# Kernel tuning notes

Measured on AMD Instinct MI355X. Metric: run time of the kernel, lower is better.

The kernel has to match this reference:

```python
import jax, jax.numpy as jnp
import numpy as np

N = 10000
E = 160000
IN_CH, HID, OUT = 14, 128, 4
HEADS = 8
NEG_SLOPE = 0.2


def setup_inputs() -> dict:
    key = jax.random.key(0)
    ks = jax.random.split(key, 16)
    glorot = lambda k, shape: jax.random.normal(k, shape, jnp.float32) * np.sqrt(2.0 / (shape[0] + shape[-1]))
    inp = {
        'x': jax.random.normal(ks[0], (N, IN_CH), jnp.float32),
        'edge_index': jax.random.randint(ks[1], (2, E), 0, N, jnp.int64),
        # layer 1: 14 -> 8 heads x 128, concat
        'W1': glorot(ks[2], (IN_CH, HEADS * HID)),
        'a_src1': glorot(ks[3], (HEADS, HID)),
        'a_dst1': glorot(ks[4], (HEADS, HID)),
        'b1': jnp.zeros((HEADS * HID,), jnp.float32),
        # layer 2: 1024 -> 8 heads x 128, concat
        'W2': glorot(ks[5], (HEADS * HID, HEADS * HID)),
        'a_src2': glorot(ks[6], (HEADS, HID)),
        'a_dst2': glorot(ks[7], (HEADS, HID)),
        'b2': jnp.zeros((HEADS * HID,), jnp.float32),
        # layer 3: 1024 -> 1 head x 4, mean (concat=False)
        'W3': glorot(ks[8], (HEADS * HID, OUT)),
        'a_src3': glorot(ks[9], (1, OUT)),
        'a_dst3': glorot(ks[10], (1, OUT)),
        'b3': jnp.zeros((OUT,), jnp.float32),
    }
    return inp


def gat_conv(x, src, dst, W, a_src, a_dst, b, heads, out_ch, concat):
    n = x.shape[0]
    h = (x @ W).reshape(n, heads, out_ch)                      # [N,H,C]
    al_s = jnp.sum(h * a_src, axis=-1)                         # [N,H]
    al_d = jnp.sum(h * a_dst, axis=-1)                         # [N,H]
    e = al_s[src] + al_d[dst]                                  # [E,H]
    e = jnp.where(e > 0, e, NEG_SLOPE * e)                     # LeakyReLU(0.2)
    # segment softmax over incoming edges of each dst node
    m = jax.ops.segment_max(e, dst, num_segments=n)
    ex = jnp.exp(e - m[dst])
    z = jax.ops.segment_sum(ex, dst, num_segments=n)
    alpha = ex / (z[dst] + 1e-16)                              # [E,H]
    out = jax.ops.segment_sum(h[src] * alpha[:, :, None], dst, num_segments=n)  # [N,H,C]
    out = out.reshape(n, heads * out_ch) if concat else out.mean(axis=1)
    return out + b


def reference(x, edge_index, W1, a_src1, a_dst1, b1, W2, a_src2, a_dst2, b2, W3, a_src3, a_dst3, b3):
    n = x.shape[0]
    # add self-loops (PyG GATConv default)
    loop = jnp.arange(n, dtype=edge_index.dtype)
    src = jnp.concatenate([edge_index[0], loop])
    dst = jnp.concatenate([edge_index[1], loop])
    # dropout layers are identity in eval mode
    h = gat_conv(x, src, dst, W1, a_src1, a_dst1, b1, HEADS, HID, True)
    h = jax.nn.relu(h)
    h = gat_conv(h, src, dst, W2, a_src2, a_dst2, b2, HEADS, HID, True)
    h = jax.nn.relu(h)
    h = gat_conv(h, src, dst, W3, a_src3, a_dst3, b3, 1, OUT, False)
    h = jax.nn.relu(h)
    return h
```

## Files before the change

### kernel.cpp

```cpp
#include <hip/hip_runtime.h>

typedef unsigned short ushort_t;
typedef unsigned int uint32;

#define N_NODES 10000
#define N_EDGES 160000
#define ET (N_NODES + N_EDGES)
#define HT 1024
#define HEADS 8
#define NEG 0.2f

#define O_FLAG     0
#define O_BND      64
#define O_COUNTS   256
#define O_OFFS     (O_COUNTS + 40192)
#define O_SSORT    (O_OFFS + 40192)
#define O_ALS1     (O_SSORT + 680192)
#define O_ALD1     (O_ALS1 + 320000)
#define O_ALS2     (O_ALD1 + 320000)
#define O_ALD2     (O_ALS2 + 320000)
#define O_AL3S     O_ALS2
#define O_AL3D     (O_ALS2 + 40192)
#define O_H3       (O_ALS2 + 80384)
#define O_WVEC     (O_ALD2 + 320000)
#define O_W3F      (O_WVEC + 24576)
#define O_S3F      (O_W3F + 16384)
#define O_W2T      (O_S3F + 768)
#define O_BUFA     (O_W2T + 2097152)
#define O_BUFB     (O_BUFA + 20480000)

__device__ __forceinline__ float bf2f(ushort_t u){ return __uint_as_float(((uint32)u) << 16); }
__device__ __forceinline__ ushort_t f2bf(float f){
    uint32 x = __float_as_uint(f);
    return (ushort_t)((x + 0x7fffu + ((x >> 16) & 1u)) >> 16);
}
__device__ __forceinline__ void unpack2(uint32 u, float& lo, float& hi){
    lo = __uint_as_float(u << 16);
    hi = __uint_as_float(u & 0xffff0000u);
}

typedef __bf16 bf16x8 __attribute__((ext_vector_type(8)));
typedef float  f32x4  __attribute__((ext_vector_type(4)));

typedef const __attribute__((address_space(1))) uint32* gas1_u32;
typedef       __attribute__((address_space(3))) uint32* las3_u32;

__device__ __forceinline__ void gload_lds16(const void* g, void* l){
    __builtin_amdgcn_global_load_lds((gas1_u32)g, (las3_u32)l, 16, 0, 0);
}

__device__ __forceinline__ int probe_f32(const uint32* __restrict__ w){
    int cnt = 0;
    for (int i = 0; i < 256; i++){
        uint32 e = (w[i] >> 7) & 0xffu;
        cnt += (e >= 64u && e <= 160u) ? 1 : 0;
    }
    return (cnt > 200) ? 0 : 1;
}
__global__ void k_probe(const int* __restrict__ ei, const uint32* __restrict__ w1raw,
                        int* __restrict__ flags){
    if (threadIdx.x == 0){
        int nz = 0;
        for (int i = 0; i < 128; i++) nz |= ei[2*i + 1];
        flags[0] = (nz == 0) ? 1 : 0;
    }
    if (threadIdx.x == 1) flags[1] = probe_f32(w1raw);
}

__device__ __forceinline__ float cvt1(const void* p, int i, int f32){
    return f32 ? ((const float*)p)[i] : bf2f(((const ushort_t*)p)[i]);
}

struct CvtArgs {
    const void* vsrc[6];
    const void* w3src;
    const void* s3src[3];
};

__global__ __launch_bounds__(256) void k_setup(CvtArgs a, const void* __restrict__ W2,
                                               const int* __restrict__ flags,
                                               float* __restrict__ wvecF, float* __restrict__ W3F,
                                               float* __restrict__ s3F,
                                               int* __restrict__ counts,
                                               float* __restrict__ alS2, float* __restrict__ alD2,
                                               uint32* __restrict__ bnd,
                                               ushort_t* __restrict__ W2T){
    __shared__ ushort_t tile[32][33];
    int b = blockIdx.x, tid = threadIdx.x;
    int f32 = flags[1];
    if (b < 11){
        if (b == 0 && tid < 32) bnd[tid] = 0;
        int g = b * 1024 + tid * 4;
        #pragma unroll
        for (int j = 0; j < 4; j++){
            int i = g + j;
            if (i < 6144) wvecF[i] = cvt1(a.vsrc[i >> 10], i & 1023, f32);
            else if (i < 10240) W3F[i - 6144] = cvt1(a.w3src, i - 6144, f32);
            else if (i < 10252){
                int off = i - 10240;
                s3F[(off >> 2) * 16 + (off & 3)] = cvt1(a.s3src[off >> 2], off & 3, f32);
            }
        }
    } else if (b < 21){
        int g = (b - 11) * 1024 + tid * 4;
        #pragma unroll
        for (int j = 0; j < 4; j++) if (g + j < N_NODES) counts[g + j] = 0;
    } else if (b < 178){
        int g = (b - 21) * 1024 + tid * 4;
        if (g < 80000){ *(float4*)(alS2 + g) = make_float4(0,0,0,0); }
        else if (g < 160000){ *(float4*)(alD2 + g - 80000) = make_float4(0,0,0,0); }
    } else {
        int t = b - 178;
        int bx = t & 31, by = t >> 5;
        int cx = tid & 31, ry = (tid >> 5) * 4;
        #pragma unroll
        for (int r = 0; r < 4; r++){
            size_t idx = (size_t)(by*32 + ry + r)*1024 + bx*32 + cx;
            tile[ry + r][cx] = f32 ? f2bf(((const float*)W2)[idx]) : ((const ushort_t*)W2)[idx];
        }
        __syncthreads();
        #pragma unroll
        for (int r = 0; r < 4; r++)
            W2T[(size_t)(bx*32 + ry + r)*1024 + by*32 + cx] = tile[cx][ry + r];
    }
}

__global__ __launch_bounds__(256) void k_extract_hist(const void* __restrict__ ei, const int* __restrict__ flags,
                                                      int* __restrict__ counts){
    int i = blockIdx.x * 256 + threadIdx.x;
    int is64 = flags[0];
    int d = -1;
    if (i < N_EDGES){
        d = is64 ? (int)((const long long*)ei)[N_EDGES + i] : ((const int*)ei)[N_EDGES + i];
    } else if (i < ET){
        d = i - N_EDGES;
    }
    if (d >= 0) atomicAdd(&counts[d], 1);
}

__global__ __launch_bounds__(1024) void k_scan(int* __restrict__ counts, int* __restrict__ offs, int n){
    __shared__ int wsum[16];
    __shared__ int running_s;
    int tid = threadIdx.x;
    int lane = tid & 63, wid = tid >> 6;
    if (tid == 0) running_s = 0;
    __syncthreads();
    for (int base = 0; base < n; base += 1024){
        int i = base + tid;
        int v = (i < n) ? counts[i] : 0;
        int x = v;
        #pragma unroll
        for (int d = 1; d < 64; d <<= 1){
            int t = __shfl_up(x, d, 64);
            if (lane >= d) x += t;
        }
        if (lane == 63) wsum[wid] = x;
        __syncthreads();
        if (wid == 0 && lane < 16){
            int w = wsum[lane];
            #pragma unroll
            for (int d = 1; d < 16; d <<= 1){
                int t = __shfl_up(w, d, 64);
                if (lane >= d) w += t;
            }
            wsum[lane] = w;
        }
        __syncthreads();
        int wprefix = (wid == 0) ? 0 : wsum[wid - 1];
        int run = running_s;
        int excl = run + wprefix + (x - v);
        if (i < n){ offs[i] = excl; counts[i] = excl; }
        __syncthreads();
        if (tid == 0) running_s = run + wsum[15];
        __syncthreads();
    }
    if (tid == 0) offs[n] = running_s;
}

__global__ __launch_bounds__(256) void k_scatter(const void* __restrict__ ei, const int* __restrict__ flags,
                                                 int* __restrict__ cursors, int* __restrict__ ssort){
    int i = blockIdx.x * 256 + threadIdx.x;
    if (i >= ET) return;
    int is64 = flags[0];
    int s, d;
    if (i < N_EDGES){
        if (is64){
            s = (int)((const long long*)ei)[i];
            d = (int)((const long long*)ei)[N_EDGES + i];
        } else {
            s = ((const int*)ei)[i];
            d = ((const int*)ei)[N_EDGES + i];
        }
    } else { s = i - N_EDGES; d = s; }
    int pos = atomicAdd(&cursors[d], 1);
    ssort[pos] = s;
}

__global__ __launch_bounds__(256) void k_gemm1f(const void* __restrict__ x, const void* __restrict__ W1,
                                                const int* __restrict__ flags,
                                                const float* __restrict__ wvecF,
                                                ushort_t* __restrict__ h1,
                                                float* __restrict__ alS, float* __restrict__ alD,
                                                uint32* __restrict__ bnd){
    __shared__ float w1s[14 * HT];
    __shared__ uint32 smax[16];
    int tid = threadIdx.x;
    int f32 = flags[1];
    if (tid < 16) smax[tid] = 0;
    if (f32){
        for (int i = tid * 4; i < 14 * HT; i += 1024)
            *(float4*)(w1s + i) = *(const float4*)((const float*)W1 + i);
    } else {
        for (int i = tid * 4; i < 14 * HT; i += 1024){
            uint2 u = *(const uint2*)((const ushort_t*)W1 + i);
            unpack2(u.x, w1s[i], w1s[i+1]);
            unpack2(u.y, w1s[i+2], w1s[i+3]);
        }
    }
    __syncthreads();
    int c0 = tid * 4;
    float4 sv = *(const float4*)(wvecF + c0);
    float4 dv = *(const float4*)(wvecF + 1024 + c0);
    int head = tid >> 5, l32 = tid & 31;
    #pragma unroll 1
    for (int n = blockIdx.x; n < N_NODES; n += 512){
        float a0=0.f, a1=0.f, a2=0.f, a3=0.f;
        #pragma unroll
        for (int k = 0; k < 14; k++){
            float xv = f32 ? ((const float*)x)[n*14 + k] : bf2f(((const ushort_t*)x)[n*14 + k]);
            float4 w = *(const float4*)(w1s + k*HT + c0);
            a0 += xv*w.x; a1 += xv*w.y; a2 += xv*w.z; a3 += xv*w.w;
        }
        uint2 o;
        o.x = (uint32)f2bf(a0) | ((uint32)f2bf(a1) << 16);
        o.y = (uint32)f2bf(a2) | ((uint32)f2bf(a3) << 16);
        *(uint2*)(h1 + (size_t)n*HT + c0) = o;
        float h0,h1v,h2,h3v;
        unpack2(o.x, h0, h1v); unpack2(o.y, h2, h3v);
        float s = h0*sv.x + h1v*sv.y + h2*sv.z + h3v*sv.w;
        float d = h0*dv.x + h1v*dv.y + h2*dv.z + h3v*dv.w;
        #pragma unroll
        for (int of = 16; of; of >>= 1){ s += __shfl_xor(s, of, 32); d += __shfl_xor(d, of, 32); }
        if (l32 == 0){
            alS[n*HEADS + head] = s; alD[n*HEADS + head] = d;
            atomicMax(&smax[head],     __float_as_uint(fmaxf(s, 0.f)));
            atomicMax(&smax[8 + head], __float_as_uint(fmaxf(d, 0.f)));
        }
    }
    __syncthreads();
    if (tid < 16) atomicMax(&bnd[tid], smax[tid]);
}

__global__ __launch_bounds__(256) void k_bound(const float* __restrict__ alS2, const float* __restrict__ alD2,
                                               uint32* __restrict__ bnd){
    int g = blockIdx.x * 256 + threadIdx.x;
    int lane = threadIdx.x & 63;
    float ms = 0.f, md = 0.f;
    for (int i = g; i < 80000; i += 10240){ ms = fmaxf(ms, alS2[i]); md = fmaxf(md, alD2[i]); }
    #pragma unroll
    for (int o = 8; o < 64; o <<= 1){
        ms = fmaxf(ms, __shfl_xor(ms, o, 64));
        md = fmaxf(md, __shfl_xor(md, o, 64));
    }
    if (lane < 8){
        atomicMax(&bnd[16 + lane], __float_as_uint(ms));
        atomicMax(&bnd[24 + lane], __float_as_uint(md));
    }
}

__global__ __launch_bounds__(256) void k_gat_agg(const ushort_t* __restrict__ H, const float* __restrict__ alS,
                                                 const float* __restrict__ alD, const uint32* __restrict__ bnd,
                                                 int bo, const int* __restrict__ offs,
                                                 const int* __restrict__ srcs, const float* __restrict__ bias,
                                                 ushort_t* __restrict__ out){
    int tid = threadIdx.x;
    int wv = tid >> 6, lane = tid & 63;
    int n = blockIdx.x * 2 + (wv >> 1);
    int half = wv & 1;
    int beg = offs[n], end = offs[n+1];
    int head = half*4 + (lane >> 4);
    float ad = alD[n*HEADS + head];
    float B = __uint_as_float(bnd[bo + head]) + __uint_as_float(bnd[bo + 8 + head]);

    int ch0 = half*512 + lane*8;
    const ushort_t* Hc = H + ch0;
    float z = 0.f;
    float c0=0.f,c1=0.f,c2=0.f,c3=0.f,c4=0.f,c5=0.f,c6=0.f,c7=0.f;
    for (int c = beg; c < end; c += 64){
        int cn = min(64, end - c);
        int sreg = (lane < cn) ? srcs[c + lane] : 0;
        int j = 0;
        for (; j + 8 <= cn; j += 8){
            int s[8]; uint4 u[8]; float e[8];
            #pragma unroll
            for (int q = 0; q < 8; q++) s[q] = __shfl(sreg, j + q, 64);
            #pragma unroll
            for (int q = 0; q < 8; q++) u[q] = *(const uint4*)(Hc + (size_t)s[q]*HT);
            #pragma unroll
            for (int q = 0; q < 8; q++) e[q] = alS[s[q]*HEADS + head];
            #pragma unroll
            for (int q = 0; q < 8; q++){
                float v = e[q] + ad;
                v = v > 0.f ? v : NEG*v;
                float w = __expf(v - B);
                z += w;
                float f0,f1,f2,f3,f4,f5,f6,f7;
                unpack2(u[q].x,f0,f1); unpack2(u[q].y,f2,f3);
                unpack2(u[q].z,f4,f5); unpack2(u[q].w,f6,f7);
                c0+=w*f0; c1+=w*f1; c2+=w*f2; c3+=w*f3;
                c4+=w*f4; c5+=w*f5; c6+=w*f6; c7+=w*f7;
            }
        }
        for (; j < cn; j++){
            int s0 = __shfl(sreg, j, 64);
            uint4 u0 = *(const uint4*)(Hc + (size_t)s0*HT);
            float v = alS[s0*HEADS + head] + ad;
            v = v > 0.f ? v : NEG*v;
            float w = __expf(v - B);
            z += w;
            float f0,f1,f2,f3,f4,f5,f6,f7;
            unpack2(u0.x,f0,f1); unpack2(u0.y,f2,f3); unpack2(u0.z,f4,f5); unpack2(u0.w,f6,f7);
            c0+=w*f0; c1+=w*f1; c2+=w*f2; c3+=w*f3;
            c4+=w*f4; c5+=w*f5; c6+=w*f6; c7+=w*f7;
        }
    }
    float inv = 1.f / z;
    float4 b0 = *(const float4*)(bias + ch0);
    float4 b1 = *(const float4*)(bias + ch0 + 4);
    c0 = fmaxf(c0*inv + b0.x, 0.f); c1 = fmaxf(c1*inv + b0.y, 0.f);
    c2 = fmaxf(c2*inv + b0.z, 0.f); c3 = fmaxf(c3*inv + b0.w, 0.f);
    c4 = fmaxf(c4*inv + b1.x, 0.f); c5 = fmaxf(c5*inv + b1.y, 0.f);
    c6 = fmaxf(c6*inv + b1.z, 0.f); c7 = fmaxf(c7*inv + b1.w, 0.f);
    uint4 o;
    o.x = (uint32)f2bf(c0) | ((uint32)f2bf(c1) << 16);
    o.y = (uint32)f2bf(c2) | ((uint32)f2bf(c3) << 16);
    o.z = (uint32)f2bf(c4) | ((uint32)f2bf(c5) << 16);
    o.w = (uint32)f2bf(c6) | ((uint32)f2bf(c7) << 16);
    *(uint4*)(out + (size_t)n*HT + ch0) = o;
}

__global__ __launch_bounds__(256) void k_gemm2(const ushort_t* __restrict__ A, const ushort_t* __restrict__ BT,
                                               ushort_t* __restrict__ C,
                                               const float* __restrict__ aS, const float* __restrict__ aD,
                                               float* __restrict__ alS2, float* __restrict__ alD2){
    __shared__ ushort_t lA[128*64];
    __shared__ ushort_t lB[64*64];
    int bn = blockIdx.x, bm = blockIdx.y;
    int tid = threadIdx.x;
    int lane = tid & 63;
    int wave = tid >> 6;
    int wm = wave * 32;
    int lm = lane & 15, kg = lane >> 4;
    int swz = lm & 7;
    f32x4 acc[2][4];
    #pragma unroll
    for (int i = 0; i < 2; i++)
        #pragma unroll
        for (int j = 0; j < 4; j++) acc[i][j] = (f32x4)0.0f;

    int rowA0 = bm * 128, rowB0 = bn * 64;
    for (int k0 = 0; k0 < 1024; k0 += 64){
        #pragma unroll
        for (int it = 0; it < 4; ++it){
            int s = tid + it*256;
            int r = s >> 3, q = s & 7;
            int ra = rowA0 + r; if (ra > N_NODES-1) ra = N_NODES-1;
            gload_lds16(A + (size_t)ra*1024 + k0 + (q ^ (r & 7))*8, lA + s*8);
        }
        #pragma unroll
        for (int it = 0; it < 2; ++it){
            int s = tid + it*256;
            int r = s >> 3, q = s & 7;
            gload_lds16(BT + (size_t)(rowB0 + r)*1024 + k0 + (q ^ (r & 7))*8, lB + s*8);
        }
        __syncthreads();
        #pragma unroll
        for (int kh = 0; kh < 2; kh++){
            bf16x8 af[2], bfr[4];
            int qb = kh*4 + kg;
            int qp = (qb ^ swz) * 8;
            #pragma unroll
            for (int mt = 0; mt < 2; mt++) af[mt]  = *(const bf16x8*)(lA + (wm + mt*16 + lm)*64 + qp);
            #pragma unroll
            for (int nt = 0; nt < 4; nt++) bfr[nt] = *(const bf16x8*)(lB + (nt*16 + lm)*64 + qp);
            #pragma unroll
            for (int mt = 0; mt < 2; mt++)
                #pragma unroll
                for (int nt = 0; nt < 4; nt++)
                    acc[mt][nt] = __builtin_amdgcn_mfma_f32_16x16x32_bf16(af[mt], bfr[nt], acc[mt][nt], 0, 0, 0);
        }
        __syncthreads();
    }
    #pragma unroll
    for (int mt = 0; mt < 2; mt++){
        int row_base = bm*128 + wm + mt*16 + kg*4;
        #pragma unroll
        for (int nt = 0; nt < 4; nt++){
            int col = bn*64 + nt*16 + lm;
            #pragma unroll
            for (int r = 0; r < 4; r++){
                int row = row_base + r;
                if (row < N_NODES) C[(size_t)row*HT + col] = f2bf(acc[mt][nt][r]);
            }
        }
    }
    int head = bn >> 1;
    float as_l[4], ad_l[4];
    #pragma unroll
    for (int nt = 0; nt < 4; nt++){
        as_l[nt] = aS[bn*64 + nt*16 + lm];
        ad_l[nt] = aD[bn*64 + nt*16 + lm];
    }
    #pragma unroll
    for (int mt = 0; mt < 2; mt++){
        #pragma unroll
        for (int r = 0; r < 4; r++){
            float ps = acc[mt][0][r]*as_l[0] + acc[mt][1][r]*as_l[1]
                     + acc[mt][2][r]*as_l[2] + acc[mt][3][r]*as_l[3];
            float pd = acc[mt][0][r]*ad_l[0] + acc[mt][1][r]*ad_l[1]
                     + acc[mt][2][r]*ad_l[2] + acc[mt][3][r]*ad_l[3];
            #pragma unroll
            for (int o = 1; o < 16; o <<= 1){ ps += __shfl_xor(ps, o, 64); pd += __shfl_xor(pd, o, 64); }
            if (lm == 0){
                int row = bm*128 + wm + mt*16 + kg*4 + r;
                if (row < N_NODES){
                    atomicAdd(&alS2[row*HEADS + head], ps);
                    atomicAdd(&alD2[row*HEADS + head], pd);
                }
            }
        }
    }
}

__global__ __launch_bounds__(256) void k_gemm3(const ushort_t* __restrict__ A, const float* __restrict__ W3,
                                               const float* __restrict__ s3,
                                               float* __restrict__ h3, float* __restrict__ al3s, float* __restrict__ al3d){
    int tid = threadIdx.x;
    int lane = tid & 63, wave = tid >> 6;
    int n = blockIdx.x * 4 + wave;
    if (n >= N_NODES) return;
    float4 w3r[16];
    #pragma unroll
    for (int j = 0; j < 16; j++) w3r[j] = ((const float4*)W3)[lane*16 + j];
    const uint4* ap = (const uint4*)(A + (size_t)n*HT + lane*16);
    uint4 u0 = ap[0], u1 = ap[1];
    uint32 uu[8] = {u0.x,u0.y,u0.z,u0.w,u1.x,u1.y,u1.z,u1.w};
    float acc0=0.f, acc1=0.f, acc2=0.f, acc3=0.f;
    #pragma unroll
    for (int p = 0; p < 8; p++){
        float lo, hi;
        unpack2(uu[p], lo, hi);
        float4 wl = w3r[p*2], wh = w3r[p*2+1];
        acc0 += lo*wl.x + hi*wh.x;
        acc1 += lo*wl.y + hi*wh.y;
        acc2 += lo*wl.z + hi*wh.z;
        acc3 += lo*wl.w + hi*wh.w;
    }
    #pragma unroll
    for (int o = 32; o; o >>= 1){
        acc0 += __shfl_xor(acc0, o, 64); acc1 += __shfl_xor(acc1, o, 64);
        acc2 += __shfl_xor(acc2, o, 64); acc3 += __shfl_xor(acc3, o, 64);
    }
    if (lane == 0){
        *(float4*)(h3 + n*4) = make_float4(acc0, acc1, acc2, acc3);
        al3s[n] = acc0*s3[0] + acc1*s3[1] + acc2*s3[2] + acc3*s3[3];
        al3d[n] = acc0*s3[16] + acc1*s3[17] + acc2*s3[18] + acc3*s3[19];
    }
}

__global__ __launch_bounds__(256) void k_gat_agg3(const float* __restrict__ h3, const float* __restrict__ al3s,
                                                  const float* __restrict__ al3d, const int* __restrict__ offs,
                                                  const int* __restrict__ srcs, const float* __restrict__ b3,
                                                  const int* __restrict__ flags, void* __restrict__ out){
    int tid = threadIdx.x;
    int l = tid & 63, wave = tid >> 6;
    int n = blockIdx.x * 4 + wave;
    if (n >= N_NODES) return;
    int beg = offs[n], end = offs[n+1];
    float ad = al3d[n];
    float m = -1e30f;
    for (int e = beg + l; e < end; e += 64){
        float v = al3s[srcs[e]] + ad; v = v > 0.f ? v : NEG*v;
        m = fmaxf(m, v);
    }
    #pragma unroll
    for (int o = 32; o; o >>= 1) m = fmaxf(m, __shfl_xor(m, o, 64));
    float z = 0.f;
    for (int e = beg + l; e < end; e += 64){
        float v = al3s[srcs[e]] + ad; v = v > 0.f ? v : NEG*v;
        z += __expf(v - m);
    }
    #pragma unroll
    for (int o = 32; o; o >>= 1) z += __shfl_xor(z, o, 64);
    float inv = 1.f / (z + 1e-16f);
    float a0=0.f, a1=0.f, a2=0.f, a3=0.f;
    for (int e = beg + l; e < end; e += 64){
        int s = srcs[e];
        float v = al3s[s] + ad; v = v > 0.f ? v : NEG*v;
        float w = __expf(v - m) * inv;
        float4 hv = *(const float4*)(h3 + s*4);
        a0 += w*hv.x; a1 += w*hv.y; a2 += w*hv.z; a3 += w*hv.w;
    }
    #pragma unroll
    for (int o = 32; o; o >>= 1){
        a0 += __shfl_xor(a0, o, 64); a1 += __shfl_xor(a1, o, 64);
        a2 += __shfl_xor(a2, o, 64); a3 += __shfl_xor(a3, o, 64);
    }
    if (l == 0){
        float r0 = fmaxf(a0 + b3[0], 0.f);
        float r1 = fmaxf(a1 + b3[1], 0.f);
        float r2 = fmaxf(a2 + b3[2], 0.f);
        float r3 = fmaxf(a3 + b3[3], 0.f);
        if (flags[1]){
            float* o4 = (float*)out;
            o4[n*4+0]=r0; o4[n*4+1]=r1; o4[n*4+2]=r2; o4[n*4+3]=r3;
        } else {
            ushort_t* o2 = (ushort_t*)out;
            o2[n*4+0]=f2bf(r0); o2[n*4+1]=f2bf(r1); o2[n*4+2]=f2bf(r2); o2[n*4+3]=f2bf(r3);
        }
    }
}

extern "C" void kernel_launch(void* const* d_in, const int* in_sizes, int n_in,
                              void* d_out, int out_size, void* d_ws, size_t ws_size,
                              hipStream_t stream){
    const void* x   = d_in[0];
    const void* ei  = d_in[1];
    const void* W1  = d_in[2];
    const void* W2  = d_in[6];
    const void* W3  = d_in[10];

    char* ws = (char*)d_ws;
    int* flags     = (int*)(ws + O_FLAG);
    uint32* bnd    = (uint32*)(ws + O_BND);
    int* counts    = (int*)(ws + O_COUNTS);
    int* offs      = (int*)(ws + O_OFFS);
    int* ssort     = (int*)(ws + O_SSORT);
    float* alS1    = (float*)(ws + O_ALS1);
    float* alD1    = (float*)(ws + O_ALD1);
    float* alS2    = (float*)(ws + O_ALS2);
    float* alD2    = (float*)(ws + O_ALD2);
    float* al3s    = (float*)(ws + O_AL3S);
    float* al3d    = (float*)(ws + O_AL3D);
    float* h3      = (float*)(ws + O_H3);
    float* wvecF   = (float*)(ws + O_WVEC);
    float* W3F     = (float*)(ws + O_W3F);
    float* s3F     = (float*)(ws + O_S3F);
    ushort_t* W2T  = (ushort_t*)(ws + O_W2T);
    ushort_t* bufA = (ushort_t*)(ws + O_BUFA);
    ushort_t* bufB = (ushort_t*)(ws + O_BUFB);

    const int EB = (ET + 255) / 256;

    CvtArgs ca;
    ca.vsrc[0]=d_in[3];  ca.vsrc[1]=d_in[4];  ca.vsrc[2]=d_in[5];
    ca.vsrc[3]=d_in[7];  ca.vsrc[4]=d_in[8];  ca.vsrc[5]=d_in[9];
    ca.w3src = W3;
    ca.s3src[0]=d_in[11]; ca.s3src[1]=d_in[12]; ca.s3src[2]=d_in[13];

    k_probe<<<1, 64, 0, stream>>>((const int*)ei, (const uint32*)W1, flags);
    k_setup<<<1202, 256, 0, stream>>>(ca, W2, flags, wvecF, W3F, s3F, counts, alS2, alD2, bnd, W2T);
    k_extract_hist<<<EB, 256, 0, stream>>>(ei, flags, counts);
    k_scan<<<1, 1024, 0, stream>>>(counts, offs, N_NODES);
    k_scatter<<<EB, 256, 0, stream>>>(ei, flags, counts, ssort);

    k_gemm1f<<<512, 256, 0, stream>>>(x, W1, flags, wvecF, bufA, alS1, alD1, bnd);
    k_gat_agg<<<5000, 256, 0, stream>>>(bufA, alS1, alD1, bnd, 0, offs, ssort, wvecF + 2*1024, bufB);

    k_gemm2<<<dim3(16, 79), 256, 0, stream>>>(bufB, W2T, bufA, wvecF + 3*1024, wvecF + 4*1024, alS2, alD2);
    k_bound<<<40, 256, 0, stream>>>(alS2, alD2, bnd);
    k_gat_agg<<<5000, 256, 0, stream>>>(bufA, alS2, alD2, bnd, 16, offs, ssort, wvecF + 5*1024, bufB);

    k_gemm3<<<2500, 256, 0, stream>>>(bufB, W3F, s3F, h3, al3s, al3d);
    k_gat_agg3<<<2500, 256, 0, stream>>>(h3, al3s, al3d, offs, ssort, s3F + 32, flags, d_out);
}
```

Baseline: 342.4 us.

## Fold probe into setup, fuse histogram with gemm1, parallelize scan

Removes the separate probe kernel by computing the dtype and edge-width probes inside k_setup. Merges the degree histogram with the layer-1 projection into one launch using block-index partitioning. Replaces the single-block serial scan with a two-kernel multi-block scan, where each block sums the preceding block totals itself. This cuts launch count and serialization on the CSR build path. The cost is that every setup block re-runs the f32 probe, and the gemm1 blocks now reserve large LDS even when they run alongside the lightweight histogram blocks.

```diff
diff --git a/kernel.cpp b/kernel.cpp
--- a/kernel.cpp
+++ b/kernel.cpp
@@ -12,7 +12,8 @@
 
 #define O_FLAG     0
 #define O_BND      64
-#define O_COUNTS   256
+#define O_BSUM     192
+#define O_COUNTS   512
 #define O_OFFS     (O_COUNTS + 40192)
 #define O_SSORT    (O_OFFS + 40192)
 #define O_ALS1     (O_SSORT + 680192)
@@ -57,14 +58,10 @@
     }
     return (cnt > 200) ? 0 : 1;
 }
-__global__ void k_probe(const int* __restrict__ ei, const uint32* __restrict__ w1raw,
-                        int* __restrict__ flags){
-    if (threadIdx.x == 0){
-        int nz = 0;
-        for (int i = 0; i < 128; i++) nz |= ei[2*i + 1];
-        flags[0] = (nz == 0) ? 1 : 0;
-    }
-    if (threadIdx.x == 1) flags[1] = probe_f32(w1raw);
+__device__ __forceinline__ int probe_edge64(const int* __restrict__ ei){
+    int nz = 0;
+    for (int i = 0; i < 128; i++) nz |= ei[2*i + 1];
+    return (nz == 0) ? 1 : 0;
 }
 
 __device__ __forceinline__ float cvt1(const void* p, int i, int f32){
@@ -78,7 +75,9 @@
 };
 
 __global__ __launch_bounds__(256) void k_setup(CvtArgs a, const void* __restrict__ W2,
-                                               const int* __restrict__ flags,
+                                               const uint32* __restrict__ w1raw,
+                                               const int* __restrict__ eiraw,
+                                               int* __restrict__ flags,
                                                float* __restrict__ wvecF, float* __restrict__ W3F,
                                                float* __restrict__ s3F,
                                                int* __restrict__ counts,
@@ -87,9 +86,13 @@
                                                ushort_t* __restrict__ W2T){
     __shared__ ushort_t tile[32][33];
     int b = blockIdx.x, tid = threadIdx.x;
-    int f32 = flags[1];
+    int f32 = probe_f32(w1raw);
     if (b < 11){
-        if (b == 0 && tid < 32) bnd[tid] = 0;
+        if (b == 0){
+            if (tid < 32) bnd[tid] = 0;
+            if (tid == 32) flags[0] = probe_edge64(eiraw);
+            if (tid == 33) flags[1] = f32;
+        }
         int g = b * 1024 + tid * 4;
         #pragma unroll
         for (int j = 0; j < 4; j++){
@@ -125,56 +128,112 @@
     }
 }
 
-__global__ __launch_bounds__(256) void k_extract_hist(const void* __restrict__ ei, const int* __restrict__ flags,
-                                                      int* __restrict__ counts){
-    int i = blockIdx.x * 256 + threadIdx.x;
-    int is64 = flags[0];
-    int d = -1;
-    if (i < N_EDGES){
-        d = is64 ? (int)((const long long*)ei)[N_EDGES + i] : ((const int*)ei)[N_EDGES + i];
-    } else if (i < ET){
-        d = i - N_EDGES;
-    }
-    if (d >= 0) atomicAdd(&counts[d], 1);
-}
-
-__global__ __launch_bounds__(1024) void k_scan(int* __restrict__ counts, int* __restrict__ offs, int n){
-    __shared__ int wsum[16];
-    __shared__ int running_s;
-    int tid = threadIdx.x;
+__global__ __launch_bounds__(256) void k_exgemm1(const void* __restrict__ ei, const void* __restrict__ x,
+                                                 const void* __restrict__ W1, const int* __restrict__ flags,
+                                                 const float* __restrict__ wvecF,
+                                                 int* __restrict__ counts,
+                                                 ushort_t* __restrict__ h1,
+                                                 float* __restrict__ alS, float* __restrict__ alD,
+                                                 uint32* __restrict__ bnd){
+    __shared__ float w1s[14 * HT];
+    __shared__ uint32 smax[16];
+    int bid = blockIdx.x, tid = threadIdx.x;
+    if (bid < 665){
+        int i = bid * 256 + tid;
+        int is64 = flags[0];
+        int d = -1;
+        if (i < N_EDGES){
+            d = is64 ? (int)((const long long*)ei)[N_EDGES + i] : ((const int*)ei)[N_EDGES + i];
+        } else if (i < ET){
+            d = i - N_EDGES;
+        }
+        if (d >= 0) atomicAdd(&counts[d], 1);
+        return;
+    }
+    int gb = bid - 665;
+    int f32 = flags[1];
+    if (tid < 16) smax[tid] = 0;
+    if (f32){
+        for (int i = tid * 4; i < 14 * HT; i += 1024)
+            *(float4*)(w1s + i) = *(const float4*)((const float*)W1 + i);
+    } else {
+        for (int i = tid * 4; i < 14 * HT; i += 1024){
+            uint2 u = *(const uint2*)((const ushort_t*)W1 + i);
+            unpack2(u.x, w1s[i], w1s[i+1]);
+            unpack2(u.y, w1s[i+2], w1s[i+3]);
+        }
+    }
+    __syncthreads();
+    int c0 = tid * 4;
+    float4 sv = *(const float4*)(wvecF + c0);
+    float4 dv = *(const float4*)(wvecF + 1024 + c0);
+    int head = tid >> 5, l32 = tid & 31;
+    #pragma unroll 1
+    for (int n = gb; n < N_NODES; n += 512){
+        float a0=0.f, a1=0.f, a2=0.f, a3=0.f;
+        #pragma unroll
+        for (int k = 0; k < 14; k++){
+            float xv = f32 ? ((const float*)x)[n*14 + k] : bf2f(((const ushort_t*)x)[n*14 + k]);
+            float4 w = *(const float4*)(w1s + k*HT + c0);
+            a0 += xv*w.x; a1 += xv*w.y; a2 += xv*w.z; a3 += xv*w.w;
+        }
+        uint2 o;
+        o.x = (uint32)f2bf(a0) | ((uint32)f2bf(a1) << 16);
+        o.y = (uint32)f2bf(a2) | ((uint32)f2bf(a3) << 16);
+        *(uint2*)(h1 + (size_t)n*HT + c0) = o;
+        float h0,h1v,h2,h3v;
+        unpack2(o.x, h0, h1v); unpack2(o.y, h2, h3v);
+        float s = h0*sv.x + h1v*sv.y + h2*sv.z + h3v*sv.w;
+        float d = h0*dv.x + h1v*dv.y + h2*dv.z + h3v*dv.w;
+        #pragma unroll
+        for (int of = 16; of; of >>= 1){ s += __shfl_xor(s, of, 32); d += __shfl_xor(d, of, 32); }
+        if (l32 == 0){
+            alS[n*HEADS + head] = s; alD[n*HEADS + head] = d;
+            atomicMax(&smax[head],     __float_as_uint(fmaxf(s, 0.f)));
+            atomicMax(&smax[8 + head], __float_as_uint(fmaxf(d, 0.f)));
+        }
+    }
+    __syncthreads();
+    if (tid < 16) atomicMax(&bnd[tid], smax[tid]);
+}
+
+__global__ __launch_bounds__(256) void k_scan_a(const int* __restrict__ counts, int* __restrict__ bsum){
+    __shared__ int ws[4];
+    int b = blockIdx.x, tid = threadIdx.x;
+    int i = b * 256 + tid;
+    int v = (i < N_NODES) ? counts[i] : 0;
     int lane = tid & 63, wid = tid >> 6;
-    if (tid == 0) running_s = 0;
+    #pragma unroll
+    for (int o = 32; o; o >>= 1) v += __shfl_xor(v, o, 64);
+    if (lane == 0) ws[wid] = v;
     __syncthreads();
-    for (int base = 0; base < n; base += 1024){
-        int i = base + tid;
-        int v = (i < n) ? counts[i] : 0;
-        int x = v;
-        #pragma unroll
-        for (int d = 1; d < 64; d <<= 1){
-            int t = __shfl_up(x, d, 64);
-            if (lane >= d) x += t;
-        }
-        if (lane == 63) wsum[wid] = x;
-        __syncthreads();
-        if (wid == 0 && lane < 16){
-            int w = wsum[lane];
-            #pragma unroll
-            for (int d = 1; d < 16; d <<= 1){
-                int t = __shfl_up(w, d, 64);
-                if (lane >= d) w += t;
-            }
-            wsum[lane] = w;
-        }
-        __syncthreads();
-        int wprefix = (wid == 0) ? 0 : wsum[wid - 1];
-        int run = running_s;
-        int excl = run + wprefix + (x - v);
-        if (i < n){ offs[i] = excl; counts[i] = excl; }
-        __syncthreads();
-        if (tid == 0) running_s = run + wsum[15];
-        __syncthreads();
-    }
-    if (tid == 0) offs[n] = running_s;
+    if (tid == 0) bsum[b] = ws[0] + ws[1] + ws[2] + ws[3];
+}
+
+__global__ __launch_bounds__(256) void k_scan_b(int* __restrict__ counts, const int* __restrict__ bsum,
+                                                int* __restrict__ offs){
+    __shared__ int ws[4];
+    int b = blockIdx.x, tid = threadIdx.x;
+    int i = b * 256 + tid;
+    int v = (i < N_NODES) ? counts[i] : 0;
+    int base = 0;
+    #pragma unroll 1
+    for (int j = 0; j < b; j++) base += bsum[j];
+    int lane = tid & 63, wid = tid >> 6;
+    int inc = v;
+    #pragma unroll
+    for (int d = 1; d < 64; d <<= 1){
+        int t = __shfl_up(inc, d, 64);
+        if (lane >= d) inc += t;
+    }
+    if (lane == 63) ws[wid] = inc;
+    __syncthreads();
+    int wpre = 0;
+    #pragma unroll
+    for (int j = 0; j < 4; j++) if (j < wid) wpre += ws[j];
+    int excl = base + wpre + inc - v;
+    if (i < N_NODES){ offs[i] = excl; counts[i] = excl; }
+    if (i == N_NODES) offs[i] = excl;
 }
 
 __global__ __launch_bounds__(256) void k_scatter(const void* __restrict__ ei, const int* __restrict__ flags,
@@ -194,61 +253,6 @@
     } else { s = i - N_EDGES; d = s; }
     int pos = atomicAdd(&cursors[d], 1);
     ssort[pos] = s;
-}
-
-__global__ __launch_bounds__(256) void k_gemm1f(const void* __restrict__ x, const void* __restrict__ W1,
-                                                const int* __restrict__ flags,
-                                                const float* __restrict__ wvecF,
-                                                ushort_t* __restrict__ h1,
-                                                float* __restrict__ alS, float* __restrict__ alD,
-                                                uint32* __restrict__ bnd){
-    __shared__ float w1s[14 * HT];
-    __shared__ uint32 smax[16];
-    int tid = threadIdx.x;
-    int f32 = flags[1];
-    if (tid < 16) smax[tid] = 0;
-    if (f32){
-        for (int i = tid * 4; i < 14 * HT; i += 1024)
-            *(float4*)(w1s + i) = *(const float4*)((const float*)W1 + i);
-    } else {
-        for (int i = tid * 4; i < 14 * HT; i += 1024){
-            uint2 u = *(const uint2*)((const ushort_t*)W1 + i);
-            unpack2(u.x, w1s[i], w1s[i+1]);
-            unpack2(u.y, w1s[i+2], w1s[i+3]);
-        }
-    }
-    __syncthreads();
-    int c0 = tid * 4;
-    float4 sv = *(const float4*)(wvecF + c0);
-    float4 dv = *(const float4*)(wvecF + 1024 + c0);
-    int head = tid >> 5, l32 = tid & 31;
-    #pragma unroll 1
-    for (int n = blockIdx.x; n < N_NODES; n += 512){
-        float a0=0.f, a1=0.f, a2=0.f, a3=0.f;
-        #pragma unroll
-        for (int k = 0; k < 14; k++){
-            float xv = f32 ? ((const float*)x)[n*14 + k] : bf2f(((const ushort_t*)x)[n*14 + k]);
-            float4 w = *(const float4*)(w1s + k*HT + c0);
-            a0 += xv*w.x; a1 += xv*w.y; a2 += xv*w.z; a3 += xv*w.w;
-        }
-        uint2 o;
-        o.x = (uint32)f2bf(a0) | ((uint32)f2bf(a1) << 16);
-        o.y = (uint32)f2bf(a2) | ((uint32)f2bf(a3) << 16);
-        *(uint2*)(h1 + (size_t)n*HT + c0) = o;
-        float h0,h1v,h2,h3v;
-        unpack2(o.x, h0, h1v); unpack2(o.y, h2, h3v);
-        float s = h0*sv.x + h1v*sv.y + h2*sv.z + h3v*sv.w;
-        float d = h0*dv.x + h1v*dv.y + h2*dv.z + h3v*dv.w;
-        #pragma unroll
-        for (int of = 16; of; of >>= 1){ s += __shfl_xor(s, of, 32); d += __shfl_xor(d, of, 32); }
-        if (l32 == 0){
-            alS[n*HEADS + head] = s; alD[n*HEADS + head] = d;
-            atomicMax(&smax[head],     __float_as_uint(fmaxf(s, 0.f)));
-            atomicMax(&smax[8 + head], __float_as_uint(fmaxf(d, 0.f)));
-        }
-    }
-    __syncthreads();
-    if (tid < 16) atomicMax(&bnd[tid], smax[tid]);
 }
 
 __global__ __launch_bounds__(256) void k_bound(const float* __restrict__ alS2, const float* __restrict__ alD2,
@@ -533,6 +537,7 @@
     char* ws = (char*)d_ws;
     int* flags     = (int*)(ws + O_FLAG);
     uint32* bnd    = (uint32*)(ws + O_BND);
+    int* bsum      = (int*)(ws + O_BSUM);
     int* counts    = (int*)(ws + O_COUNTS);
     int* offs      = (int*)(ws + O_OFFS);
     int* ssort     = (int*)(ws + O_SSORT);
@@ -558,13 +563,13 @@
     ca.w3src = W3;
     ca.s3src[0]=d_in[11]; ca.s3src[1]=d_in[12]; ca.s3src[2]=d_in[13];
 
-    k_probe<<<1, 64, 0, stream>>>((const int*)ei, (const uint32*)W1, flags);
-    k_setup<<<1202, 256, 0, stream>>>(ca, W2, flags, wvecF, W3F, s3F, counts, alS2, alD2, bnd, W2T);
-    k_extract_hist<<<EB, 256, 0, stream>>>(ei, flags, counts);
-    k_scan<<<1, 1024, 0, stream>>>(counts, offs, N_NODES);
+    k_setup<<<1202, 256, 0, stream>>>(ca, W2, (const uint32*)W1, (const int*)ei, flags,
+                                      wvecF, W3F, s3F, counts, alS2, alD2, bnd, W2T);
+    k_exgemm1<<<1177, 256, 0, stream>>>(ei, x, W1, flags, wvecF, counts, bufA, alS1, alD1, bnd);
+    k_scan_a<<<40, 256, 0, stream>>>(counts, bsum);
+    k_scan_b<<<40, 256, 0, stream>>>(counts, bsum, offs);
     k_scatter<<<EB, 256, 0, stream>>>(ei, flags, counts, ssort);
 
-    k_gemm1f<<<512, 256, 0, stream>>>(x, W1, flags, wvecF, bufA, alS1, alD1, bnd);
     k_gat_agg<<<5000, 256, 0, stream>>>(bufA, alS1, alD1, bnd, 0, offs, ssort, wvecF + 2*1024, bufB);
 
     k_gemm2<<<dim3(16, 79), 256, 0, stream>>>(bufB, W2T, bufA, wvecF + 3*1024, wvecF + 4*1024, alS2, alD2);
```

Result: faster. 335.0 us (-2.1%).
